# Kernel optimization log

Measured on AMD Instinct MI355X. Metric: run time of the kernel, lower is better.

## Reference

```python
import jax, jax.numpy as jnp
import numpy as np

ANGLE_BINS = 16
RADIUS_BINS = 8


def _bilinear_cart(img, ys, xs):
    # img [B,C,H,W]; ys/xs: sample grid [A,R] in pixel coords, zero outside image
    h, w = img.shape[2], img.shape[3]
    y0 = jnp.floor(ys)
    x0 = jnp.floor(xs)
    wy = (ys - y0).astype(img.dtype)
    wx = (xs - x0).astype(img.dtype)
    y0i = jnp.clip(y0, 0, h - 1).astype(jnp.int32)
    y1i = jnp.clip(y0 + 1, 0, h - 1).astype(jnp.int32)
    x0i = jnp.clip(x0, 0, w - 1).astype(jnp.int32)
    x1i = jnp.clip(x0 + 1, 0, w - 1).astype(jnp.int32)
    v00 = img[:, :, y0i, x0i]
    v01 = img[:, :, y0i, x1i]
    v10 = img[:, :, y1i, x0i]
    v11 = img[:, :, y1i, x1i]
    out = (v00 * (1 - wy) * (1 - wx) + v01 * (1 - wy) * wx
           + v10 * wy * (1 - wx) + v11 * wy * wx)
    valid = ((ys >= 0) & (ys <= h - 1) & (xs >= 0) & (xs <= w - 1)).astype(img.dtype)
    return out * valid


def cartesian_to_polar(x):
    # [B,C,H,W] -> [B,C,ANGLE_BINS,RADIUS_BINS] via bilinear sampling on a polar grid
    b, c, h, w = x.shape
    cy = (h - 1) / 2.0
    cx = (w - 1) / 2.0
    max_r = min(h, w) / 2.0
    theta = 2.0 * jnp.pi * jnp.arange(ANGLE_BINS, dtype=jnp.float32) / ANGLE_BINS
    r = (jnp.arange(RADIUS_BINS, dtype=jnp.float32) + 0.5) / RADIUS_BINS * max_r
    ys = cy + r[None, :] * jnp.sin(theta)[:, None]  # [A,R]
    xs = cx + r[None, :] * jnp.cos(theta)[:, None]  # [A,R]
    return _bilinear_cart(x, ys, xs)


def polar_to_cartesian(pf, h, w):
    # [B,C,A,R] -> [B,C,H,W]: inverse remap with angular wrap, radial clamp,
    # zero outside the max radius disc
    b, c, A, R = pf.shape
    cy = (h - 1) / 2.0
    cx = (w - 1) / 2.0
    max_r = min(h, w) / 2.0
    yy, xx = jnp.meshgrid(jnp.arange(h, dtype=jnp.float32),
                          jnp.arange(w, dtype=jnp.float32), indexing='ij')
    dy = yy - cy
    dx = xx - cx
    rr = jnp.sqrt(dy * dy + dx * dx)
    th = jnp.mod(jnp.arctan2(dy, dx), 2.0 * jnp.pi)
    a = th / (2.0 * jnp.pi) * A
    ri = rr / max_r * R - 0.5
    a0 = jnp.floor(a)
    wa = (a - a0).astype(pf.dtype)
    a0i = jnp.mod(a0.astype(jnp.int32), A)
    a1i = jnp.mod(a0i + 1, A)
    r0 = jnp.floor(ri)
    wr = (ri - r0).astype(pf.dtype)
    r0i = jnp.clip(r0, 0, R - 1).astype(jnp.int32)
    r1i = jnp.clip(r0 + 1, 0, R - 1).astype(jnp.int32)
    v00 = pf[:, :, a0i, r0i]
    v01 = pf[:, :, a0i, r1i]
    v10 = pf[:, :, a1i, r0i]
    v11 = pf[:, :, a1i, r1i]
    out = (v00 * (1 - wa) * (1 - wr) + v01 * (1 - wa) * wr
           + v10 * wa * (1 - wr) + v11 * wa * wr)
    valid = (rr <= max_r).astype(pf.dtype)
    return out * valid


def setup_inputs() -> dict:
    key = jax.random.key(0)
    ks = jax.random.split(key, 4)
    B, C, H, W = 16, 256, 128, 128
    x = jax.random.normal(ks[0], (B, C, H, W), dtype=jnp.float32)
    # grouped 3x3 conv: groups=4 -> kernel [C_out=C, C_in/groups=C//4, 3, 3]
    w_polar = jax.random.normal(ks[1], (C, C // 4, 3, 3), dtype=jnp.float32) * 0.05
    b_polar = jnp.zeros((C,), jnp.float32)
    w_attn1 = jax.random.normal(ks[2], (C // 4, C), dtype=jnp.float32) * 0.05
    b_attn1 = jnp.zeros((C // 4,), jnp.float32)
    w_attn2 = jax.random.normal(ks[3], (1, C // 4), dtype=jnp.float32) * 0.05
    b_attn2 = jnp.zeros((1,), jnp.float32)
    return {"x": x, "w_polar": w_polar, "b_polar": b_polar,
            "w_attn1": w_attn1, "b_attn1": b_attn1,
            "w_attn2": w_attn2, "b_attn2": b_attn2}


def reference(x, w_polar, b_polar, w_attn1, b_attn1, w_attn2, b_attn2):
    b, c, h, w = x.shape
    pf = cartesian_to_polar(x)  # [B,C,16,8]
    pp = jax.lax.conv_general_dilated(
        pf, w_polar, window_strides=(1, 1), padding=((1, 1), (1, 1)),
        dimension_numbers=('NCHW', 'OIHW', 'NCHW'), feature_group_count=4)
    pp = pp + b_polar[None, :, None, None]
    pc = polar_to_cartesian(pp, h, w)  # [B,C,H,W]
    h1 = jax.nn.relu(jnp.einsum('bchw,oc->bohw', pc, w_attn1)
                     + b_attn1[None, :, None, None])
    att = jax.nn.sigmoid(jnp.einsum('bchw,oc->bohw', h1, w_attn2)
                         + b_attn2[None, :, None, None])  # [B,1,H,W]
    return x * att
```

## Files before the change

### kernel.cpp

```cpp
#include <hip/hip_runtime.h>
#include <math.h>

#define TWO_PI 6.28318530717958647692f

__global__ __launch_bounds__(256) void k1_cart2polar(const float* __restrict__ x,
                                                     float* __restrict__ pf) {
    int t = blockIdx.x * 256 + threadIdx.x;
    int r = t & 7;
    int a = (t >> 3) & 15;
    int c = (t >> 7) & 255;
    int b = t >> 15;
    float theta = (TWO_PI * (float)a) / 16.0f;
    float rad   = ((float)r + 0.5f) / 8.0f * 64.0f;
    float ys = 63.5f + rad * sinf(theta);
    float xs = 63.5f + rad * cosf(theta);
    float y0 = floorf(ys), x0 = floorf(xs);
    float wy = ys - y0,    wx = xs - x0;
    int y0i = min(max((int)y0, 0), 127);
    int y1i = min(max((int)y0 + 1, 0), 127);
    int x0i = min(max((int)x0, 0), 127);
    int x1i = min(max((int)x0 + 1, 0), 127);
    const float* img = x + ((size_t)(b * 256 + c) << 14);
    float v00 = img[y0i * 128 + x0i];
    float v01 = img[y0i * 128 + x1i];
    float v10 = img[y1i * 128 + x0i];
    float v11 = img[y1i * 128 + x1i];
    float v = v00 * (1.0f - wy) * (1.0f - wx) + v01 * (1.0f - wy) * wx
            + v10 * wy * (1.0f - wx)          + v11 * wy * wx;
    float valid = (ys >= 0.0f && ys <= 127.0f && xs >= 0.0f && xs <= 127.0f) ? 1.0f : 0.0f;
    pf[t] = v * valid;
}

__global__ __launch_bounds__(128) void k2_conv(const float* __restrict__ pf,
                                               const float* __restrict__ w_polar,
                                               const float* __restrict__ b_polar,
                                               float* __restrict__ pp_t) {
    __shared__ __align__(16) float pfs[64 * 180];
    int bid = blockIdx.x;
    int b  = bid >> 5;
    int g  = (bid >> 3) & 3;
    int ot = bid & 7;
    int tid = threadIdx.x;
    for (int i = tid; i < 64 * 180; i += 128) pfs[i] = 0.0f;
    __syncthreads();
    const float* src = pf + ((size_t)(b * 256 + g * 64) << 7);
    for (int i = tid; i < 8192; i += 128) {
        int ic = i >> 7, bin = i & 127;
        int a = bin >> 3, r = bin & 7;
        pfs[ic * 180 + (a + 1) * 10 + (r + 1)] = src[i];
    }
    __syncthreads();

    int a = tid >> 3, r = tid & 7;
    int oc0 = g * 64 + ot * 8;
    float acc[8];
    #pragma unroll
    for (int j = 0; j < 8; ++j) acc[j] = b_polar[oc0 + j];

    for (int ic = 0; ic < 64; ++ic) {
        float v[9];
        const float* base = pfs + ic * 180 + a * 10 + r;
        #pragma unroll
        for (int dh = 0; dh < 3; ++dh)
            #pragma unroll
            for (int dw = 0; dw < 3; ++dw)
                v[dh * 3 + dw] = base[dh * 10 + dw];
        #pragma unroll
        for (int j = 0; j < 8; ++j) {
            const float* wp = w_polar + ((size_t)(oc0 + j) * 64 + (size_t)ic) * 9;
            acc[j] += wp[0]*v[0] + wp[1]*v[1] + wp[2]*v[2]
                    + wp[3]*v[3] + wp[4]*v[4] + wp[5]*v[5]
                    + wp[6]*v[6] + wp[7]*v[7] + wp[8]*v[8];
        }
    }
    float* dst = pp_t + ((size_t)((b << 7) + tid)) * 256 + oc0;
    #pragma unroll
    for (int j = 0; j < 8; ++j) dst[j] = acc[j];
}

__global__ __launch_bounds__(256) void k3_proj(const float* __restrict__ pp_t,
                                               const float* __restrict__ w_attn1,
                                               float* __restrict__ q) {
    __shared__ __align__(16) float wl[16384];
    int tid = threadIdx.x;
    for (int i = tid; i < 16384; i += 256) {
        int o = i >> 8, c = i & 255;
        wl[(c << 6) + (o ^ (c & 31))] = w_attn1[i];
    }
    __syncthreads();
    int n = blockIdx.x * 256 + tid;
    int b   = n >> 13;
    int bin = (n >> 6) & 127;
    int o   = n & 63;
    const float4* pr4 = (const float4*)(pp_t + ((size_t)((b << 7) + bin)) * 256);
    float acc = 0.0f;
    #pragma unroll 8
    for (int c4 = 0; c4 < 64; ++c4) {
        float4 p = pr4[c4];
        int c = c4 << 2;
        acc += wl[( c      << 6) + (o ^ ( c      & 31))] * p.x;
        acc += wl[((c + 1) << 6) + (o ^ ((c + 1) & 31))] * p.y;
        acc += wl[((c + 2) << 6) + (o ^ ((c + 2) & 31))] * p.z;
        acc += wl[((c + 3) << 6) + (o ^ ((c + 3) & 31))] * p.w;
    }
    q[n] = acc;
}

__global__ __launch_bounds__(256) void k4a_att(const float* __restrict__ q,
                                               const float* __restrict__ b_attn1,
                                               const float* __restrict__ w_attn2,
                                               const float* __restrict__ b_attn2,
                                               float* __restrict__ att) {
    __shared__ __align__(16) float qs[8896];
    __shared__ __align__(16) float b1s[64];
    __shared__ __align__(16) float w2s[64];
    int b    = blockIdx.x >> 6;
    int tile = blockIdx.x & 63;
    int tid  = threadIdx.x;
    const float* qb = q + ((size_t)b << 13);
    for (int i = tid; i < 8192; i += 256) {
        int bin = i >> 6, o = i & 63;
        qs[(bin >> 3) * 556 + (bin & 7) * 68 + o] = qb[i];
    }
    if (tid < 64) { b1s[tid] = b_attn1[tid]; w2s[tid] = w_attn2[tid]; }
    __syncthreads();
    float b2 = b_attn2[0];
    const float4* q4  = (const float4*)qs;
    const float4* b14 = (const float4*)b1s;
    const float4* w24 = (const float4*)w2s;

    int p = (tile << 8) + tid;
    int h = p >> 7, w = p & 127;
    float dy = (float)h - 63.5f;
    float dx = (float)w - 63.5f;
    float rr = sqrtf(dy * dy + dx * dx);
    float th = atan2f(dy, dx);
    if (th < 0.0f) th += TWO_PI;
    float aa = th / TWO_PI * 16.0f;
    float a0 = floorf(aa);
    float wa = aa - a0;
    int ia0 = ((int)a0) & 15;
    int ia1 = (ia0 + 1) & 15;
    float ri = rr / 64.0f * 8.0f - 0.5f;
    float r0 = floorf(ri);
    float wr = ri - r0;
    int ir0 = (int)fminf(fmaxf(r0, 0.0f), 7.0f);
    int ir1 = (int)fminf(fmaxf(r0 + 1.0f, 0.0f), 7.0f);
    float valid = (rr <= 64.0f) ? 1.0f : 0.0f;
    float w00 = valid * (1.0f - wa) * (1.0f - wr);
    float w01 = valid * (1.0f - wa) * wr;
    float w10 = valid * wa * (1.0f - wr);
    float w11 = valid * wa * wr;
    int t00 = ia0 * 139 + ir0 * 17;
    int t01 = ia0 * 139 + ir1 * 17;
    int t10 = ia1 * 139 + ir0 * 17;
    int t11 = ia1 * 139 + ir1 * 17;
    float acc = b2;
    #pragma unroll
    for (int i = 0; i < 16; ++i) {
        float4 v00 = q4[t00 + i], v01 = q4[t01 + i];
        float4 v10 = q4[t10 + i], v11 = q4[t11 + i];
        float4 bb = b14[i], ww = w24[i];
        float sx = w00 * v00.x + w01 * v01.x + w10 * v10.x + w11 * v11.x;
        float sy = w00 * v00.y + w01 * v01.y + w10 * v10.y + w11 * v11.y;
        float sz = w00 * v00.z + w01 * v01.z + w10 * v10.z + w11 * v11.z;
        float sw = w00 * v00.w + w01 * v01.w + w10 * v10.w + w11 * v11.w;
        acc += fmaxf(sx + bb.x, 0.0f) * ww.x;
        acc += fmaxf(sy + bb.y, 0.0f) * ww.y;
        acc += fmaxf(sz + bb.z, 0.0f) * ww.z;
        acc += fmaxf(sw + bb.w, 0.0f) * ww.w;
    }
    float attv = 1.0f / (1.0f + expf(-acc));
    att[((size_t)b << 14) + p] = attv;
}

__global__ __launch_bounds__(256) void k4b_mul(const float4* __restrict__ x4,
                                               const float* __restrict__ att,
                                               float4* __restrict__ out4) {
    const float4* att4 = (const float4*)att;
    int idx = blockIdx.x * 256 + threadIdx.x;
    int stride = gridDim.x * 256;
    for (int i = idx; i < 16777216; i += stride) {
        float4 xv = x4[i];
        float4 av = att4[((i >> 20) << 12) | (i & 4095)];
        out4[i] = make_float4(xv.x * av.x, xv.y * av.y, xv.z * av.z, xv.w * av.w);
    }
}

extern "C" void kernel_launch(void* const* d_in, const int* in_sizes, int n_in,
                              void* d_out, int out_size, void* d_ws, size_t ws_size,
                              hipStream_t stream) {
    const float* x       = (const float*)d_in[0];
    const float* w_polar = (const float*)d_in[1];
    const float* b_polar = (const float*)d_in[2];
    const float* w_attn1 = (const float*)d_in[3];
    const float* b_attn1 = (const float*)d_in[4];
    const float* w_attn2 = (const float*)d_in[5];
    const float* b_attn2 = (const float*)d_in[6];
    float* out = (float*)d_out;
    float* ws  = (float*)d_ws;

    float* pf   = ws;
    float* pp_t = ws + 524288;
    float* q    = ws + 1048576;
    float* att  = ws + 1179648;

    hipLaunchKernelGGL(k1_cart2polar, dim3(2048), dim3(256), 0, stream, x, pf);
    hipLaunchKernelGGL(k2_conv,       dim3(512),  dim3(128), 0, stream, pf, w_polar, b_polar, pp_t);
    hipLaunchKernelGGL(k3_proj,       dim3(512),  dim3(256), 0, stream, pp_t, w_attn1, q);
    hipLaunchKernelGGL(k4a_att,       dim3(1024), dim3(256), 0, stream, q, b_attn1, w_attn2, b_attn2, att);
    hipLaunchKernelGGL(k4b_mul,       dim3(2048), dim3(256), 0, stream,
                       (const float4*)x, att, (float4*)out);
}
```

Baseline: 180.0 us.

## Precompute polar sample tables, split conv input channels, use nontemporal elementwise IO

The cart-to-polar kernel now computes the 128 bilinear offsets and weights once per block in shared memory instead of recomputing trig per element. The grouped polar conv uses 256 threads that split the input channels in half and reduce the two partial sums through shared memory. The final multiply uses nontemporal load and store of x and out to avoid polluting cache with streaming data, and the sigmoid switches to fast __expf. These target per-thread redundant math, conv latency and cache pressure in the dominant bandwidth-bound multiply.

```diff
diff --git a/kernel.cpp b/kernel.cpp
--- a/kernel.cpp
+++ b/kernel.cpp
@@ -3,63 +3,80 @@
 
 #define TWO_PI 6.28318530717958647692f
 
+typedef float f4 __attribute__((ext_vector_type(4)));
+
 __global__ __launch_bounds__(256) void k1_cart2polar(const float* __restrict__ x,
                                                      float* __restrict__ pf) {
-    int t = blockIdx.x * 256 + threadIdx.x;
-    int r = t & 7;
-    int a = (t >> 3) & 15;
-    int c = (t >> 7) & 255;
-    int b = t >> 15;
-    float theta = (TWO_PI * (float)a) / 16.0f;
-    float rad   = ((float)r + 0.5f) / 8.0f * 64.0f;
-    float ys = 63.5f + rad * sinf(theta);
-    float xs = 63.5f + rad * cosf(theta);
-    float y0 = floorf(ys), x0 = floorf(xs);
-    float wy = ys - y0,    wx = xs - x0;
-    int y0i = min(max((int)y0, 0), 127);
-    int y1i = min(max((int)y0 + 1, 0), 127);
-    int x0i = min(max((int)x0, 0), 127);
-    int x1i = min(max((int)x0 + 1, 0), 127);
-    const float* img = x + ((size_t)(b * 256 + c) << 14);
-    float v00 = img[y0i * 128 + x0i];
-    float v01 = img[y0i * 128 + x1i];
-    float v10 = img[y1i * 128 + x0i];
-    float v11 = img[y1i * 128 + x1i];
-    float v = v00 * (1.0f - wy) * (1.0f - wx) + v01 * (1.0f - wy) * wx
-            + v10 * wy * (1.0f - wx)          + v11 * wy * wx;
-    float valid = (ys >= 0.0f && ys <= 127.0f && xs >= 0.0f && xs <= 127.0f) ? 1.0f : 0.0f;
-    pf[t] = v * valid;
-}
-
-__global__ __launch_bounds__(128) void k2_conv(const float* __restrict__ pf,
+    __shared__ float w00s[128], w01s[128], w10s[128], w11s[128];
+    __shared__ int   o00s[128], o01s[128], o10s[128], o11s[128];
+    int tid = threadIdx.x;
+    if (tid < 128) {
+        int a = tid >> 3, r = tid & 7;
+        float theta = (TWO_PI * (float)a) / 16.0f;
+        float rad   = ((float)r + 0.5f) / 8.0f * 64.0f;
+        float ys = 63.5f + rad * sinf(theta);
+        float xs = 63.5f + rad * cosf(theta);
+        float y0 = floorf(ys), x0 = floorf(xs);
+        float wy = ys - y0,    wx = xs - x0;
+        int y0i = min(max((int)y0, 0), 127);
+        int y1i = min(max((int)y0 + 1, 0), 127);
+        int x0i = min(max((int)x0, 0), 127);
+        int x1i = min(max((int)x0 + 1, 0), 127);
+        float valid = (ys >= 0.0f && ys <= 127.0f && xs >= 0.0f && xs <= 127.0f) ? 1.0f : 0.0f;
+        w00s[tid] = valid * (1.0f - wy) * (1.0f - wx);
+        w01s[tid] = valid * (1.0f - wy) * wx;
+        w10s[tid] = valid * wy * (1.0f - wx);
+        w11s[tid] = valid * wy * wx;
+        o00s[tid] = y0i * 128 + x0i;
+        o01s[tid] = y0i * 128 + x1i;
+        o10s[tid] = y1i * 128 + x0i;
+        o11s[tid] = y1i * 128 + x1i;
+    }
+    __syncthreads();
+    int t = blockIdx.x * 256 + tid;
+    int bin = t & 127;
+    int img = t >> 7;
+    const float* ib = x + ((size_t)img << 14);
+    float v = ib[o00s[bin]] * w00s[bin]
+            + ib[o01s[bin]] * w01s[bin]
+            + ib[o10s[bin]] * w10s[bin]
+            + ib[o11s[bin]] * w11s[bin];
+    pf[t] = v;
+}
+
+__global__ __launch_bounds__(256) void k2_conv(const float* __restrict__ pf,
                                                const float* __restrict__ w_polar,
                                                const float* __restrict__ b_polar,
                                                float* __restrict__ pp_t) {
     __shared__ __align__(16) float pfs[64 * 180];
+    __shared__ __align__(16) float red[128 * 8];
     int bid = blockIdx.x;
     int b  = bid >> 5;
     int g  = (bid >> 3) & 3;
     int ot = bid & 7;
     int tid = threadIdx.x;
-    for (int i = tid; i < 64 * 180; i += 128) pfs[i] = 0.0f;
+    for (int i = tid; i < 64 * 180; i += 256) pfs[i] = 0.0f;
     __syncthreads();
     const float* src = pf + ((size_t)(b * 256 + g * 64) << 7);
-    for (int i = tid; i < 8192; i += 128) {
+    for (int i = tid; i < 8192; i += 256) {
         int ic = i >> 7, bin = i & 127;
-        int a = bin >> 3, r = bin & 7;
-        pfs[ic * 180 + (a + 1) * 10 + (r + 1)] = src[i];
-    }
-    __syncthreads();
-
-    int a = tid >> 3, r = tid & 7;
+        pfs[ic * 180 + ((bin >> 3) + 1) * 10 + (bin & 7) + 1] = src[i];
+    }
+    __syncthreads();
+
+    int half = tid >> 7;
+    int bt   = tid & 127;
+    int a = bt >> 3, r = bt & 7;
     int oc0 = g * 64 + ot * 8;
     float acc[8];
     #pragma unroll
-    for (int j = 0; j < 8; ++j) acc[j] = b_polar[oc0 + j];
-
-    for (int ic = 0; ic < 64; ++ic) {
+    for (int j = 0; j < 8; ++j) acc[j] = 0.0f;
+
+    const float* wbase = w_polar + (size_t)oc0 * 576 + half * 288;
+    const float* pbase = pfs + half * 32 * 180 + a * 10 + r;
+    for (int ic = 0; ic < 32; ++ic) {
         float v[9];
-        const float* base = pfs + ic * 180 + a * 10 + r;
+        const float* base = pbase + ic * 180;
         #pragma unroll
         for (int dh = 0; dh < 3; ++dh)
             #pragma unroll
@@ -67,15 +84,23 @@
                 v[dh * 3 + dw] = base[dh * 10 + dw];
         #pragma unroll
         for (int j = 0; j < 8; ++j) {
-            const float* wp = w_polar + ((size_t)(oc0 + j) * 64 + (size_t)ic) * 9;
+            const float* wp = wbase + j * 576 + ic * 9;
             acc[j] += wp[0]*v[0] + wp[1]*v[1] + wp[2]*v[2]
                     + wp[3]*v[3] + wp[4]*v[4] + wp[5]*v[5]
                     + wp[6]*v[6] + wp[7]*v[7] + wp[8]*v[8];
         }
     }
-    float* dst = pp_t + ((size_t)((b << 7) + tid)) * 256 + oc0;
-    #pragma unroll
-    for (int j = 0; j < 8; ++j) dst[j] = acc[j];
+    if (half) {
+        #pragma unroll
+        for (int j = 0; j < 8; ++j) red[bt * 8 + j] = acc[j];
+    }
+    __syncthreads();
+    if (!half) {
+        float* dst = pp_t + ((size_t)((b << 7) + bt)) * 256 + oc0;
+        #pragma unroll
+        for (int j = 0; j < 8; ++j)
+            dst[j] = acc[j] + red[bt * 8 + j] + b_polar[oc0 + j];
+    }
 }
 
 __global__ __launch_bounds__(256) void k3_proj(const float* __restrict__ pp_t,
@@ -170,20 +195,20 @@
         acc += fmaxf(sz + bb.z, 0.0f) * ww.z;
         acc += fmaxf(sw + bb.w, 0.0f) * ww.w;
     }
-    float attv = 1.0f / (1.0f + expf(-acc));
+    float attv = 1.0f / (1.0f + __expf(-acc));
     att[((size_t)b << 14) + p] = attv;
 }
 
-__global__ __launch_bounds__(256) void k4b_mul(const float4* __restrict__ x4,
+__global__ __launch_bounds__(256) void k4b_mul(const f4* __restrict__ x4,
                                                const float* __restrict__ att,
-                                               float4* __restrict__ out4) {
-    const float4* att4 = (const float4*)att;
+                                               f4* __restrict__ out4) {
+    const f4* att4 = (const f4*)att;
     int idx = blockIdx.x * 256 + threadIdx.x;
     int stride = gridDim.x * 256;
     for (int i = idx; i < 16777216; i += stride) {
-        float4 xv = x4[i];
-        float4 av = att4[((i >> 20) << 12) | (i & 4095)];
-        out4[i] = make_float4(xv.x * av.x, xv.y * av.y, xv.z * av.z, xv.w * av.w);
+        f4 xv = __builtin_nontemporal_load(&x4[i]);
+        f4 av = att4[((i >> 20) << 12) | (i & 4095)];
+        __builtin_nontemporal_store(xv * av, &out4[i]);
     }
 }
 
@@ -206,9 +231,9 @@
     float* att  = ws + 1179648;
 
     hipLaunchKernelGGL(k1_cart2polar, dim3(2048), dim3(256), 0, stream, x, pf);
-    hipLaunchKernelGGL(k2_conv,       dim3(512),  dim3(128), 0, stream, pf, w_polar, b_polar, pp_t);
+    hipLaunchKernelGGL(k2_conv,       dim3(512),  dim3(256), 0, stream, pf, w_polar, b_polar, pp_t);
     hipLaunchKernelGGL(k3_proj,       dim3(512),  dim3(256), 0, stream, pp_t, w_attn1, q);
     hipLaunchKernelGGL(k4a_att,       dim3(1024), dim3(256), 0, stream, q, b_attn1, w_attn2, b_attn2, att);
     hipLaunchKernelGGL(k4b_mul,       dim3(2048), dim3(256), 0, stream,
-                       (const float4*)x, att, (float4*)out);
-}
+                       (const f4*)x, att, (f4*)out);
+}
```

New measurement: 172.0 us. -4.4%, faster.
